# Optimization experiments

Hardware: AMD Instinct MI355X
Metric: run time of the kernel (lower is better)

The kernel has to match this reference:

```python
import jax, jax.numpy as jnp
from jax import lax
import numpy as np

B, S, I, H, O = 4096, 32, 16, 32, 1


def setup_inputs() -> dict:
    key = jax.random.key(0)
    ks = jax.random.split(key, 20)
    sc = 0.1
    inp = {
        "x": jax.random.normal(ks[0], (B, S, I), dtype=jnp.float32),
        "t": jnp.sort(jax.random.uniform(ks[1], (B, S), dtype=jnp.float32), axis=1),
        "gru_Wih": jax.random.normal(ks[2], (3 * H, I), dtype=jnp.float32) * sc,
        "gru_Whh": jax.random.normal(ks[3], (3 * H, H), dtype=jnp.float32) * sc,
        "gru_bih": jax.random.normal(ks[4], (3 * H,), dtype=jnp.float32) * sc,
        "gru_bhh": jax.random.normal(ks[5], (3 * H,), dtype=jnp.float32) * sc,
        "ode_W1": jax.random.normal(ks[6], (64, H), dtype=jnp.float32) * sc,
        "ode_b1": jax.random.normal(ks[7], (64,), dtype=jnp.float32) * sc,
        "ode_W2": jax.random.normal(ks[8], (32, 64), dtype=jnp.float32) * sc,
        "ode_b2": jax.random.normal(ks[9], (32,), dtype=jnp.float32) * sc,
        "ode_W3": jax.random.normal(ks[10], (H, 32), dtype=jnp.float32) * sc,
        "ode_b3": jax.random.normal(ks[11], (H,), dtype=jnp.float32) * sc,
        "fc_W1": jax.random.normal(ks[12], (64, H), dtype=jnp.float32) * sc,
        "fc_b1": jax.random.normal(ks[13], (64,), dtype=jnp.float32) * sc,
        "fc_W2": jax.random.normal(ks[14], (O, 64), dtype=jnp.float32) * sc,
        "fc_b2": jax.random.normal(ks[15], (O,), dtype=jnp.float32) * sc,
        "time_divs": 5,
    }
    return inp


def _forward(x, t, gru_Wih, gru_Whh, gru_bih, gru_bhh,
             ode_W1, ode_b1, ode_W2, ode_b2, ode_W3, ode_b3,
             fc_W1, fc_b1, fc_W2, fc_b2, time_divs):
    n_sub = int(time_divs) - 1  # intervals of the t_eval linspace grid

    def gru_cell(x_t, h):
        gi = x_t @ gru_Wih.T + gru_bih
        gh = h @ gru_Whh.T + gru_bhh
        i_r, i_z, i_n = jnp.split(gi, 3, axis=-1)
        h_r, h_z, h_n = jnp.split(gh, 3, axis=-1)
        r = jax.nn.sigmoid(i_r + h_r)
        z = jax.nn.sigmoid(i_z + h_z)
        n = jnp.tanh(i_n + r * h_n)
        return (1.0 - z) * n + z * h

    def ode_f(y):  # ODEFunc MLP: H -> 64 -> 32 -> H
        h1 = jax.nn.relu(y @ ode_W1.T + ode_b1)
        h2 = jax.nn.relu(h1 @ ode_W2.T + ode_b2)
        return h2 @ ode_W3.T + ode_b3

    def dopri5_step(y, dt):  # dt: (B,1); 5th-order Dormand-Prince step
        k1 = ode_f(y)
        k2 = ode_f(y + dt * (0.2 * k1))
        k3 = ode_f(y + dt * (3 / 40 * k1 + 9 / 40 * k2))
        k4 = ode_f(y + dt * (44 / 45 * k1 - 56 / 15 * k2 + 32 / 9 * k3))
        k5 = ode_f(y + dt * (19372 / 6561 * k1 - 25360 / 2187 * k2
                             + 64448 / 6561 * k3 - 212 / 729 * k4))
        k6 = ode_f(y + dt * (9017 / 3168 * k1 - 355 / 33 * k2 + 46732 / 5247 * k3
                             + 49 / 176 * k4 - 5103 / 18656 * k5))
        return y + dt * (35 / 384 * k1 + 500 / 1113 * k3 + 125 / 192 * k4
                         - 2187 / 6784 * k5 + 11 / 84 * k6)

    def step(carry, inputs):
        h, _ = carry
        x_t, dt = inputs           # x_t: (B,I), dt: (B,)
        out = gru_cell(x_t, h)     # GRU output (also candidate next hidden)
        hi = out
        ddt = (dt / n_sub)[:, None]
        for _ in range(n_sub):     # small fixed substep count, unrolled
            hi = dopri5_step(hi, ddt)
        return (hi, out), None

    bsz = x.shape[0]
    x_seq = jnp.swapaxes(x, 0, 1)[:-1]        # (S-1, B, I)
    dts = (t[:, 1:] - t[:, :-1]).T            # (S-1, B)
    h0 = jnp.zeros((bsz, gru_Whh.shape[1]), dtype=x.dtype)
    (_, out), _ = lax.scan(step, (h0, h0), (x_seq, dts))
    y = jax.nn.relu(out @ fc_W1.T + fc_b1) @ fc_W2.T + fc_b2
    return y


def reference(x, t, gru_Wih, gru_Whh, gru_bih, gru_bhh,
              ode_W1, ode_b1, ode_W2, ode_b2, ode_W3, ode_b3,
              fc_W1, fc_b1, fc_W2, fc_b2, time_divs):
    return _forward(x, t, gru_Wih, gru_Whh, gru_bih, gru_bhh,
                    ode_W1, ode_b1, ode_W2, ode_b2, ode_W3, ode_b3,
                    fc_W1, fc_b1, fc_W2, fc_b2, time_divs)
```

## Files before the change

kernel.cpp:

```cpp
#include <hip/hip_runtime.h>
#include <hip/hip_bf16.h>

#define NB 4096
#define NS 32
#define NI 16
#define NH 32

typedef float f32x2 __attribute__((ext_vector_type(2)));

__device__ __forceinline__ void fence() {
    __builtin_amdgcn_wave_barrier();
    asm volatile("s_waitcnt lgkmcnt(0)" ::: "memory");
    __builtin_amdgcn_wave_barrier();
}

__device__ __forceinline__ float xhsum(float x) {
    auto p = __builtin_amdgcn_permlane32_swap(
        (int)__float_as_uint(x), (int)__float_as_uint(x), false, false);
    return __uint_as_float((unsigned)p[0]) + __uint_as_float((unsigned)p[1]);
}

__device__ __forceinline__ f32x2 pkfma(f32x2 a, f32x2 b, f32x2 c) {
    return __builtin_elementwise_fma(a, b, c);
}

__global__ void __launch_bounds__(256)
__attribute__((amdgpu_waves_per_eu(2, 2)))
odernn_kernel(
    const float* __restrict__ x,
    const float* __restrict__ t,
    const float* __restrict__ gWih,
    const float* __restrict__ gWhh,
    const float* __restrict__ gbih,
    const float* __restrict__ gbhh,
    const float* __restrict__ oW1,
    const float* __restrict__ ob1,
    const float* __restrict__ oW2,
    const float* __restrict__ ob2,
    const float* __restrict__ oW3,
    const float* __restrict__ ob3,
    const float* __restrict__ fW1,
    const float* __restrict__ fb1,
    const float* __restrict__ fW2,
    const float* __restrict__ fb2,
    float* __restrict__ outp)
{
    const int tid  = threadIdx.x;
    const int lane = tid & 63;
    const int wid  = tid >> 6;
    const int b0   = blockIdx.x * 8 + wid * 2;
    const int b1   = b0 + 1;
    const int r    = lane & 31;
    const int hf   = lane >> 5;

    __shared__ float sWr[48 * 32];
    __shared__ float sWz[48 * 32];
    __shared__ float sWnh[32 * 32];
    __shared__ float sWni[16 * 32];
    __shared__ __align__(16) float buf[4][2][64];

    for (int i = tid; i < 48 * 32; i += 256) {
        int c = i >> 5, r0 = i & 31;
        sWr[i] = (c < 16) ? gWih[r0 * 16 + c]        : gWhh[r0 * 32 + (c - 16)];
        sWz[i] = (c < 16) ? gWih[(32 + r0) * 16 + c] : gWhh[(32 + r0) * 32 + (c - 16)];
    }
    for (int i = tid; i < 32 * 32; i += 256) {
        int c = i >> 5, r0 = i & 31;
        sWnh[i] = gWhh[(64 + r0) * 32 + c];
    }
    for (int i = tid; i < 16 * 32; i += 256) {
        int c = i >> 5, r0 = i & 31;
        sWni[i] = gWih[(64 + r0) * 16 + c];
    }
    __syncthreads();

    float* bufw0 = buf[wid][0];
    float* bufw1 = buf[wid][1];
    const float4* bb0 = reinterpret_cast<const float4*>(bufw0);
    const float4* bb1 = reinterpret_cast<const float4*>(bufw1);

    f32x2 w1_0, w1_1, w1_2, w1_3, w1_4, w1_5, w1_6, w1_7,
          w1_8, w1_9, w1_10, w1_11, w1_12, w1_13, w1_14, w1_15;
    f32x2 w2_0, w2_1, w2_2, w2_3, w2_4, w2_5, w2_6, w2_7,
          w2_8, w2_9, w2_10, w2_11, w2_12, w2_13, w2_14, w2_15;
    f32x2 w3_0, w3_1, w3_2, w3_3, w3_4, w3_5, w3_6, w3_7;
    {
        const float4* p1 = reinterpret_cast<const float4*>(oW1) + lane * 8;
        float4 v;
#define LD2(i, dA, dB) { v = p1[i]; dA = f32x2{v.x, v.y}; dB = f32x2{v.z, v.w}; }
        LD2(0, w1_0,  w1_1)  LD2(1, w1_2,  w1_3)
        LD2(2, w1_4,  w1_5)  LD2(3, w1_6,  w1_7)
        LD2(4, w1_8,  w1_9)  LD2(5, w1_10, w1_11)
        LD2(6, w1_12, w1_13) LD2(7, w1_14, w1_15)
#undef LD2
        const float4* p2 = reinterpret_cast<const float4*>(oW2) + r * 16 + hf * 8;
#define LD2(i, dA, dB) { v = p2[i]; dA = f32x2{v.x, v.y}; dB = f32x2{v.z, v.w}; }
        LD2(0, w2_0,  w2_1)  LD2(1, w2_2,  w2_3)
        LD2(2, w2_4,  w2_5)  LD2(3, w2_6,  w2_7)
        LD2(4, w2_8,  w2_9)  LD2(5, w2_10, w2_11)
        LD2(6, w2_12, w2_13) LD2(7, w2_14, w2_15)
#undef LD2
        const float4* p3 = reinterpret_cast<const float4*>(oW3) + r * 8 + hf * 4;
#define LD2(i, dA, dB) { v = p3[i]; dA = f32x2{v.x, v.y}; dB = f32x2{v.z, v.w}; }
        LD2(0, w3_0, w3_1)  LD2(1, w3_2, w3_3)
        LD2(2, w3_4, w3_5)  LD2(3, w3_6, w3_7)
#undef LD2
    }
    const float b1r = ob1[lane];
    const float b2r = ob2[r];
    const float b3r = ob3[r];

    const float brr = gbih[r]      + gbhh[r];
    const float bzz = gbih[32 + r] + gbhh[32 + r];
    const float bin = gbih[64 + r];
    const float bhn = gbhh[64 + r];

    const float* wrp  = &sWr[(hf * 24) * 32 + r];
    const float* wzp  = &sWz[(hf * 24) * 32 + r];
    const float* wnhp = &sWnh[(hf * 16) * 32 + r];
    const float* wnip = &sWni[r];

    auto ode_f2 = [&](float y0, float y1, float& o0, float& o1) {
        bufw0[hf * 32 + r] = y0;
        bufw1[hf * 32 + r] = y1;
        fence();
        f32x2 p0 = f32x2{b1r, 0.0f}, p1a = f32x2{b1r, 0.0f};
#define S1(kk, wA, wB) { float4 c0 = bb0[kk]; float4 c1 = bb1[kk]; \
        p0  = pkfma(wA, f32x2{c0.x, c0.y}, p0);  \
        p0  = pkfma(wB, f32x2{c0.z, c0.w}, p0);  \
        p1a = pkfma(wA, f32x2{c1.x, c1.y}, p1a); \
        p1a = pkfma(wB, f32x2{c1.z, c1.w}, p1a); }
        S1(0, w1_0,  w1_1)  S1(1, w1_2,  w1_3)
        S1(2, w1_4,  w1_5)  S1(3, w1_6,  w1_7)
        S1(4, w1_8,  w1_9)  S1(5, w1_10, w1_11)
        S1(6, w1_12, w1_13) S1(7, w1_14, w1_15)
#undef S1
        float a1_0 = fmaxf(p0.x + p0.y, 0.0f);
        float a1_1 = fmaxf(p1a.x + p1a.y, 0.0f);
        bufw0[lane] = a1_0;
        bufw1[lane] = a1_1;
        fence();
        f32x2 q0 = f32x2{0.0f, 0.0f}, q1 = f32x2{0.0f, 0.0f};
        const int o2 = hf * 8;
#define S2(kk, wA, wB) { float4 c0 = bb0[o2 + kk]; float4 c1 = bb1[o2 + kk]; \
        q0 = pkfma(wA, f32x2{c0.x, c0.y}, q0); \
        q0 = pkfma(wB, f32x2{c0.z, c0.w}, q0); \
        q1 = pkfma(wA, f32x2{c1.x, c1.y}, q1); \
        q1 = pkfma(wB, f32x2{c1.z, c1.w}, q1); }
        S2(0, w2_0,  w2_1)  S2(1, w2_2,  w2_3)
        S2(2, w2_4,  w2_5)  S2(3, w2_6,  w2_7)
        S2(4, w2_8,  w2_9)  S2(5, w2_10, w2_11)
        S2(6, w2_12, w2_13) S2(7, w2_14, w2_15)
#undef S2
        float a2_0 = fmaxf(xhsum(q0.x + q0.y) + b2r, 0.0f);
        float a2_1 = fmaxf(xhsum(q1.x + q1.y) + b2r, 0.0f);
        bufw0[hf * 32 + r] = a2_0;
        bufw1[hf * 32 + r] = a2_1;
        fence();
        f32x2 s0 = f32x2{0.0f, 0.0f}, s1 = f32x2{0.0f, 0.0f};
        const int o3 = hf * 4;
#define S3(kk, wA, wB) { float4 c0 = bb0[o3 + kk]; float4 c1 = bb1[o3 + kk]; \
        s0 = pkfma(wA, f32x2{c0.x, c0.y}, s0); \
        s0 = pkfma(wB, f32x2{c0.z, c0.w}, s0); \
        s1 = pkfma(wA, f32x2{c1.x, c1.y}, s1); \
        s1 = pkfma(wB, f32x2{c1.z, c1.w}, s1); }
        S3(0, w3_0, w3_1)  S3(1, w3_2, w3_3)
        S3(2, w3_4, w3_5)  S3(3, w3_6, w3_7)
#undef S3
        o0 = xhsum(s0.x + s0.y) + b3r;
        o1 = xhsum(s1.x + s1.y) + b3r;
    };

    float hv0 = 0.0f, hv1 = 0.0f;
    float outv0 = 0.0f, outv1 = 0.0f;

    #pragma unroll 1
    for (int s = 0; s < NS - 1; ++s) {
        const float* xrow0 = x + ((size_t)b0 * NS + s) * NI;
        const float* xrow1 = x + ((size_t)b1 * NS + s) * NI;
        if (hf == 0) {
            bufw0[16 + r] = hv0;
            bufw1[16 + r] = hv1;
        } else {
            bufw0[r & 15] = xrow0[r & 15];
            bufw1[r & 15] = xrow1[r & 15];
        }
        fence();

        float ar0 = 0.f, ar1 = 0.f, az0 = 0.f, az1 = 0.f;
        #pragma unroll
        for (int kk = 0; kk < 6; ++kk) {
            float4 c0 = bb0[hf*6 + kk];
            float4 c1 = bb1[hf*6 + kk];
            float w;
            w = wrp[(4*kk  )*32]; ar0 = fmaf(w, c0.x, ar0); ar1 = fmaf(w, c1.x, ar1);
            w = wrp[(4*kk+1)*32]; ar0 = fmaf(w, c0.y, ar0); ar1 = fmaf(w, c1.y, ar1);
            w = wrp[(4*kk+2)*32]; ar0 = fmaf(w, c0.z, ar0); ar1 = fmaf(w, c1.z, ar1);
            w = wrp[(4*kk+3)*32]; ar0 = fmaf(w, c0.w, ar0); ar1 = fmaf(w, c1.w, ar1);
            w = wzp[(4*kk  )*32]; az0 = fmaf(w, c0.x, az0); az1 = fmaf(w, c1.x, az1);
            w = wzp[(4*kk+1)*32]; az0 = fmaf(w, c0.y, az0); az1 = fmaf(w, c1.y, az1);
            w = wzp[(4*kk+2)*32]; az0 = fmaf(w, c0.z, az0); az1 = fmaf(w, c1.z, az1);
            w = wzp[(4*kk+3)*32]; az0 = fmaf(w, c0.w, az0); az1 = fmaf(w, c1.w, az1);
        }
        float in0 = 0.f, in1 = 0.f, hn0 = 0.f, hn1 = 0.f;
        #pragma unroll
        for (int kk = 0; kk < 4; ++kk) {
            float4 c0 = bb0[kk];
            float4 c1 = bb1[kk];
            float w;
            w = wnip[(4*kk  )*32]; in0 = fmaf(w, c0.x, in0); in1 = fmaf(w, c1.x, in1);
            w = wnip[(4*kk+1)*32]; in0 = fmaf(w, c0.y, in0); in1 = fmaf(w, c1.y, in1);
            w = wnip[(4*kk+2)*32]; in0 = fmaf(w, c0.z, in0); in1 = fmaf(w, c1.z, in1);
            w = wnip[(4*kk+3)*32]; in0 = fmaf(w, c0.w, in0); in1 = fmaf(w, c1.w, in1);
        }
        #pragma unroll
        for (int kk = 0; kk < 4; ++kk) {
            float4 c0 = bb0[4 + hf*4 + kk];
            float4 c1 = bb1[4 + hf*4 + kk];
            float w;
            w = wnhp[(4*kk  )*32]; hn0 = fmaf(w, c0.x, hn0); hn1 = fmaf(w, c1.x, hn1);
            w = wnhp[(4*kk+1)*32]; hn0 = fmaf(w, c0.y, hn0); hn1 = fmaf(w, c1.y, hn1);
            w = wnhp[(4*kk+2)*32]; hn0 = fmaf(w, c0.z, hn0); hn1 = fmaf(w, c1.z, hn1);
            w = wnhp[(4*kk+3)*32]; hn0 = fmaf(w, c0.w, hn0); hn1 = fmaf(w, c1.w, hn1);
        }
        ar0 = xhsum(ar0) + brr;  ar1 = xhsum(ar1) + brr;
        az0 = xhsum(az0) + bzz;  az1 = xhsum(az1) + bzz;
        hn0 = xhsum(hn0) + bhn;  hn1 = xhsum(hn1) + bhn;
        in0 += bin;              in1 += bin;

        float rg0 = 1.0f / (1.0f + __expf(-ar0));
        float rg1 = 1.0f / (1.0f + __expf(-ar1));
        float zg0 = 1.0f / (1.0f + __expf(-az0));
        float zg1 = 1.0f / (1.0f + __expf(-az1));
        float ng0 = tanhf(fmaf(rg0, hn0, in0));
        float ng1 = tanhf(fmaf(rg1, hn1, in1));
        outv0 = (1.0f - zg0) * ng0 + zg0 * hv0;
        outv1 = (1.0f - zg1) * ng1 + zg1 * hv1;

        hv0 = outv0;
        hv1 = outv1;
        if (s < NS - 2) {
            const float ddt0 = (t[(size_t)b0 * NS + s + 1] - t[(size_t)b0 * NS + s]) * 0.25f;
            const float ddt1 = (t[(size_t)b1 * NS + s + 1] - t[(size_t)b1 * NS + s]) * 0.25f;
            float hi0 = outv0, hi1 = outv1;
            #pragma unroll 1
            for (int sub = 0; sub < 4; ++sub) {
                float k1_0, k1_1, k2_0, k2_1, k3_0, k3_1,
                      k4_0, k4_1, k5_0, k5_1, k6_0, k6_1;
                ode_f2(hi0, hi1, k1_0, k1_1);
                ode_f2(fmaf(ddt0, 0.2f * k1_0, hi0),
                       fmaf(ddt1, 0.2f * k1_1, hi1), k2_0, k2_1);
                ode_f2(fmaf(ddt0, fmaf((float)(9.0/40.0), k2_0, (float)(3.0/40.0) * k1_0), hi0),
                       fmaf(ddt1, fmaf((float)(9.0/40.0), k2_1, (float)(3.0/40.0) * k1_1), hi1),
                       k3_0, k3_1);
                ode_f2(fmaf(ddt0, fmaf((float)(32.0/9.0), k3_0,
                                  fmaf(-(float)(56.0/15.0), k2_0, (float)(44.0/45.0) * k1_0)), hi0),
                       fmaf(ddt1, fmaf((float)(32.0/9.0), k3_1,
                                  fmaf(-(float)(56.0/15.0), k2_1, (float)(44.0/45.0) * k1_1)), hi1),
                       k4_0, k4_1);
                ode_f2(fmaf(ddt0, fmaf(-(float)(212.0/729.0), k4_0,
                                  fmaf((float)(64448.0/6561.0), k3_0,
                                  fmaf(-(float)(25360.0/2187.0), k2_0, (float)(19372.0/6561.0) * k1_0))), hi0),
                       fmaf(ddt1, fmaf(-(float)(212.0/729.0), k4_1,
                                  fmaf((float)(64448.0/6561.0), k3_1,
                                  fmaf(-(float)(25360.0/2187.0), k2_1, (float)(19372.0/6561.0) * k1_1))), hi1),
                       k5_0, k5_1);
                ode_f2(fmaf(ddt0, fmaf(-(float)(5103.0/18656.0), k5_0,
                                  fmaf((float)(49.0/176.0), k4_0,
                                  fmaf((float)(46732.0/5247.0), k3_0,
                                  fmaf(-(float)(355.0/33.0), k2_0, (float)(9017.0/3168.0) * k1_0)))), hi0),
                       fmaf(ddt1, fmaf(-(float)(5103.0/18656.0), k5_1,
                                  fmaf((float)(49.0/176.0), k4_1,
                                  fmaf((float)(46732.0/5247.0), k3_1,
                                  fmaf(-(float)(355.0/33.0), k2_1, (float)(9017.0/3168.0) * k1_1)))), hi1),
                       k6_0, k6_1);
                hi0 = fmaf(ddt0, fmaf((float)(11.0/84.0), k6_0,
                                 fmaf(-(float)(2187.0/6784.0), k5_0,
                                 fmaf((float)(125.0/192.0), k4_0,
                                 fmaf((float)(500.0/1113.0), k3_0, (float)(35.0/384.0) * k1_0)))), hi0);
                hi1 = fmaf(ddt1, fmaf((float)(11.0/84.0), k6_1,
                                 fmaf(-(float)(2187.0/6784.0), k5_1,
                                 fmaf((float)(125.0/192.0), k4_1,
                                 fmaf((float)(500.0/1113.0), k3_1, (float)(35.0/384.0) * k1_1)))), hi1);
            }
            hv0 = hi0;
            hv1 = hi1;
        }
    }

    bufw0[hf * 32 + r] = outv0;
    bufw1[hf * 32 + r] = outv1;
    fence();
    f32x2 acc0 = f32x2{fb1[lane], 0.0f};
    f32x2 acc1h = f32x2{fb1[lane], 0.0f};
    {
        const float4* fw = reinterpret_cast<const float4*>(fW1) + lane * 8;
        #pragma unroll
        for (int kk = 0; kk < 8; ++kk) {
            float4 wv = fw[kk];
            float4 c0 = bb0[kk];
            float4 c1 = bb1[kk];
            acc0  = pkfma(f32x2{wv.x, wv.y}, f32x2{c0.x, c0.y}, acc0);
            acc0  = pkfma(f32x2{wv.z, wv.w}, f32x2{c0.z, c0.w}, acc0);
            acc1h = pkfma(f32x2{wv.x, wv.y}, f32x2{c1.x, c1.y}, acc1h);
            acc1h = pkfma(f32x2{wv.z, wv.w}, f32x2{c1.z, c1.w}, acc1h);
        }
    }
    float fw2v = fW2[lane];
    float pa = fmaxf(acc0.x + acc0.y, 0.0f) * fw2v;
    float pb = fmaxf(acc1h.x + acc1h.y, 0.0f) * fw2v;
    #pragma unroll
    for (int m = 1; m < 64; m <<= 1) {
        pa += __shfl_xor(pa, m, 64);
        pb += __shfl_xor(pb, m, 64);
    }
    if (lane == 0) {
        float bias = fb2[0];
        outp[b0] = pa + bias;
        outp[b1] = pb + bias;
    }
}

extern "C" void kernel_launch(void* const* d_in, const int* in_sizes, int n_in,
                              void* d_out, int out_size, void* d_ws, size_t ws_size,
                              hipStream_t stream) {
    (void)in_sizes; (void)n_in; (void)d_ws; (void)ws_size; (void)out_size;
    odernn_kernel<<<dim3(NB / 8), dim3(256), 0, stream>>>(
        (const float*)d_in[0],  (const float*)d_in[1],
        (const float*)d_in[2],  (const float*)d_in[3],
        (const float*)d_in[4],  (const float*)d_in[5],
        (const float*)d_in[6],  (const float*)d_in[7],
        (const float*)d_in[8],  (const float*)d_in[9],
        (const float*)d_in[10], (const float*)d_in[11],
        (const float*)d_in[12], (const float*)d_in[13],
        (const float*)d_in[14], (const float*)d_in[15],
        (float*)d_out);
}
```

Measured before the change: 692.8 us.

## Repartition ODE MLP across lanes with packed two-output state and permlane reductions

The ODE MLP work is redistributed so each lane holds two output neurons packed into f32x2. The K dimension is split across half-waves and quarter-waves, and partial sums are combined with permlane16/permlane32 swaps. The RK stage combinations now run as packed FMAs on the two-element state, which removes redundant per-lane scalar stage arithmetic. The cost is extra cross-lane reductions and an LDS round trip to re-layout the hidden state before the ODE loop.

```diff
diff --git a/kernel.cpp b/kernel.cpp
--- a/kernel.cpp
+++ b/kernel.cpp
@@ -14,14 +14,22 @@
     __builtin_amdgcn_wave_barrier();
 }
 
-__device__ __forceinline__ float xhsum(float x) {
+__device__ __forceinline__ float xh32(float x) {
     auto p = __builtin_amdgcn_permlane32_swap(
         (int)__float_as_uint(x), (int)__float_as_uint(x), false, false);
     return __uint_as_float((unsigned)p[0]) + __uint_as_float((unsigned)p[1]);
 }
+__device__ __forceinline__ float xh16(float x) {
+    auto p = __builtin_amdgcn_permlane16_swap(
+        (int)__float_as_uint(x), (int)__float_as_uint(x), false, false);
+    return __uint_as_float((unsigned)p[0]) + __uint_as_float((unsigned)p[1]);
+}
 
 __device__ __forceinline__ f32x2 pkfma(f32x2 a, f32x2 b, f32x2 c) {
     return __builtin_elementwise_fma(a, b, c);
+}
+__device__ __forceinline__ f32x2 pfm(float a, f32x2 b, f32x2 c) {
+    return __builtin_elementwise_fma(f32x2{a, a}, b, c);
 }
 
 __global__ void __launch_bounds__(256)
@@ -52,6 +60,8 @@
     const int b1   = b0 + 1;
     const int r    = lane & 31;
     const int hf   = lane >> 5;
+    const int p    = lane & 15;
+    const int q    = lane >> 4;
 
     __shared__ float sWr[48 * 32];
     __shared__ float sWz[48 * 32];
@@ -81,34 +91,49 @@
 
     f32x2 w1_0, w1_1, w1_2, w1_3, w1_4, w1_5, w1_6, w1_7,
           w1_8, w1_9, w1_10, w1_11, w1_12, w1_13, w1_14, w1_15;
+    {
+        const float4* A = reinterpret_cast<const float4*>(oW1 + r * 32 + hf * 16);
+        const float4* B = reinterpret_cast<const float4*>(oW1 + (r + 32) * 32 + hf * 16);
+        float4 a, bq;
+#define LW(kk, d0, d1, d2, d3) { a = A[kk]; bq = B[kk]; \
+        d0 = f32x2{a.x, bq.x}; d1 = f32x2{a.y, bq.y}; \
+        d2 = f32x2{a.z, bq.z}; d3 = f32x2{a.w, bq.w}; }
+        LW(0, w1_0, w1_1, w1_2,  w1_3)
+        LW(1, w1_4, w1_5, w1_6,  w1_7)
+        LW(2, w1_8, w1_9, w1_10, w1_11)
+        LW(3, w1_12, w1_13, w1_14, w1_15)
+#undef LW
+    }
     f32x2 w2_0, w2_1, w2_2, w2_3, w2_4, w2_5, w2_6, w2_7,
           w2_8, w2_9, w2_10, w2_11, w2_12, w2_13, w2_14, w2_15;
+    {
+        const float4* A = reinterpret_cast<const float4*>(oW2 + p * 64 + q * 16);
+        const float4* B = reinterpret_cast<const float4*>(oW2 + (p + 16) * 64 + q * 16);
+        float4 a, bq;
+#define LW(kk, d0, d1, d2, d3) { a = A[kk]; bq = B[kk]; \
+        d0 = f32x2{a.x, bq.x}; d1 = f32x2{a.y, bq.y}; \
+        d2 = f32x2{a.z, bq.z}; d3 = f32x2{a.w, bq.w}; }
+        LW(0, w2_0, w2_1, w2_2,  w2_3)
+        LW(1, w2_4, w2_5, w2_6,  w2_7)
+        LW(2, w2_8, w2_9, w2_10, w2_11)
+        LW(3, w2_12, w2_13, w2_14, w2_15)
+#undef LW
+    }
     f32x2 w3_0, w3_1, w3_2, w3_3, w3_4, w3_5, w3_6, w3_7;
     {
-        const float4* p1 = reinterpret_cast<const float4*>(oW1) + lane * 8;
-        float4 v;
-#define LD2(i, dA, dB) { v = p1[i]; dA = f32x2{v.x, v.y}; dB = f32x2{v.z, v.w}; }
-        LD2(0, w1_0,  w1_1)  LD2(1, w1_2,  w1_3)
-        LD2(2, w1_4,  w1_5)  LD2(3, w1_6,  w1_7)
-        LD2(4, w1_8,  w1_9)  LD2(5, w1_10, w1_11)
-        LD2(6, w1_12, w1_13) LD2(7, w1_14, w1_15)
-#undef LD2
-        const float4* p2 = reinterpret_cast<const float4*>(oW2) + r * 16 + hf * 8;
-#define LD2(i, dA, dB) { v = p2[i]; dA = f32x2{v.x, v.y}; dB = f32x2{v.z, v.w}; }
-        LD2(0, w2_0,  w2_1)  LD2(1, w2_2,  w2_3)
-        LD2(2, w2_4,  w2_5)  LD2(3, w2_6,  w2_7)
-        LD2(4, w2_8,  w2_9)  LD2(5, w2_10, w2_11)
-        LD2(6, w2_12, w2_13) LD2(7, w2_14, w2_15)
-#undef LD2
-        const float4* p3 = reinterpret_cast<const float4*>(oW3) + r * 8 + hf * 4;
-#define LD2(i, dA, dB) { v = p3[i]; dA = f32x2{v.x, v.y}; dB = f32x2{v.z, v.w}; }
-        LD2(0, w3_0, w3_1)  LD2(1, w3_2, w3_3)
-        LD2(2, w3_4, w3_5)  LD2(3, w3_6, w3_7)
-#undef LD2
-    }
-    const float b1r = ob1[lane];
-    const float b2r = ob2[r];
-    const float b3r = ob3[r];
+        const float4* A = reinterpret_cast<const float4*>(oW3 + p * 32 + q * 8);
+        const float4* B = reinterpret_cast<const float4*>(oW3 + (p + 16) * 32 + q * 8);
+        float4 a, bq;
+#define LW(kk, d0, d1, d2, d3) { a = A[kk]; bq = B[kk]; \
+        d0 = f32x2{a.x, bq.x}; d1 = f32x2{a.y, bq.y}; \
+        d2 = f32x2{a.z, bq.z}; d3 = f32x2{a.w, bq.w}; }
+        LW(0, w3_0, w3_1, w3_2, w3_3)
+        LW(1, w3_4, w3_5, w3_6, w3_7)
+#undef LW
+    }
+    const f32x2 b1pk = f32x2{ob1[r], ob1[r + 32]};
+    const f32x2 b2pk = f32x2{ob2[p], ob2[p + 16]};
+    const f32x2 b3pk = f32x2{ob3[p], ob3[p + 16]};
 
     const float brr = gbih[r]      + gbhh[r];
     const float bzz = gbih[32 + r] + gbhh[32 + r];
@@ -120,78 +145,90 @@
     const float* wnhp = &sWnh[(hf * 16) * 32 + r];
     const float* wnip = &sWni[r];
 
-    auto ode_f2 = [&](float y0, float y1, float& o0, float& o1) {
-        bufw0[hf * 32 + r] = y0;
-        bufw1[hf * 32 + r] = y1;
+    const int hf4  = hf * 4;
+    const int q4   = q * 4;
+    const int q2   = q * 2;
+    const int wsel = (q & 1) << 4;
+
+    auto ode_f2 = [&](f32x2 y0, f32x2 y1, f32x2& o0, f32x2& o1) {
+        bufw0[p + wsel] = (q & 1) ? y0.y : y0.x;
+        bufw1[p + wsel] = (q & 1) ? y1.y : y1.x;
         fence();
-        f32x2 p0 = f32x2{b1r, 0.0f}, p1a = f32x2{b1r, 0.0f};
-#define S1(kk, wA, wB) { float4 c0 = bb0[kk]; float4 c1 = bb1[kk]; \
-        p0  = pkfma(wA, f32x2{c0.x, c0.y}, p0);  \
-        p0  = pkfma(wB, f32x2{c0.z, c0.w}, p0);  \
-        p1a = pkfma(wA, f32x2{c1.x, c1.y}, p1a); \
-        p1a = pkfma(wB, f32x2{c1.z, c1.w}, p1a); }
-        S1(0, w1_0,  w1_1)  S1(1, w1_2,  w1_3)
-        S1(2, w1_4,  w1_5)  S1(3, w1_6,  w1_7)
-        S1(4, w1_8,  w1_9)  S1(5, w1_10, w1_11)
-        S1(6, w1_12, w1_13) S1(7, w1_14, w1_15)
-#undef S1
-        float a1_0 = fmaxf(p0.x + p0.y, 0.0f);
-        float a1_1 = fmaxf(p1a.x + p1a.y, 0.0f);
-        bufw0[lane] = a1_0;
-        bufw1[lane] = a1_1;
+        f32x2 A0 = f32x2{0.f, 0.f}, A1 = f32x2{0.f, 0.f};
+#define S1M(kk, wA, wB, wC, wD) { \
+        float4 c0 = bb0[hf4 + kk], c1 = bb1[hf4 + kk]; \
+        A0 = pkfma(wA, f32x2{c0.x, c0.x}, A0); A1 = pkfma(wA, f32x2{c1.x, c1.x}, A1); \
+        A0 = pkfma(wB, f32x2{c0.y, c0.y}, A0); A1 = pkfma(wB, f32x2{c1.y, c1.y}, A1); \
+        A0 = pkfma(wC, f32x2{c0.z, c0.z}, A0); A1 = pkfma(wC, f32x2{c1.z, c1.z}, A1); \
+        A0 = pkfma(wD, f32x2{c0.w, c0.w}, A0); A1 = pkfma(wD, f32x2{c1.w, c1.w}, A1); }
+        S1M(0, w1_0,  w1_1,  w1_2,  w1_3)
+        S1M(1, w1_4,  w1_5,  w1_6,  w1_7)
+        S1M(2, w1_8,  w1_9,  w1_10, w1_11)
+        S1M(3, w1_12, w1_13, w1_14, w1_15)
+#undef S1M
+        f32x2 h10 = f32x2{fmaxf(xh32(A0.x) + b1pk.x, 0.f),
+                          fmaxf(xh32(A0.y) + b1pk.y, 0.f)};
+        f32x2 h11 = f32x2{fmaxf(xh32(A1.x) + b1pk.x, 0.f),
+                          fmaxf(xh32(A1.y) + b1pk.y, 0.f)};
+        bufw0[lane] = hf ? h10.y : h10.x;
+        bufw1[lane] = hf ? h11.y : h11.x;
         fence();
-        f32x2 q0 = f32x2{0.0f, 0.0f}, q1 = f32x2{0.0f, 0.0f};
-        const int o2 = hf * 8;
-#define S2(kk, wA, wB) { float4 c0 = bb0[o2 + kk]; float4 c1 = bb1[o2 + kk]; \
-        q0 = pkfma(wA, f32x2{c0.x, c0.y}, q0); \
-        q0 = pkfma(wB, f32x2{c0.z, c0.w}, q0); \
-        q1 = pkfma(wA, f32x2{c1.x, c1.y}, q1); \
-        q1 = pkfma(wB, f32x2{c1.z, c1.w}, q1); }
-        S2(0, w2_0,  w2_1)  S2(1, w2_2,  w2_3)
-        S2(2, w2_4,  w2_5)  S2(3, w2_6,  w2_7)
-        S2(4, w2_8,  w2_9)  S2(5, w2_10, w2_11)
-        S2(6, w2_12, w2_13) S2(7, w2_14, w2_15)
-#undef S2
-        float a2_0 = fmaxf(xhsum(q0.x + q0.y) + b2r, 0.0f);
-        float a2_1 = fmaxf(xhsum(q1.x + q1.y) + b2r, 0.0f);
-        bufw0[hf * 32 + r] = a2_0;
-        bufw1[hf * 32 + r] = a2_1;
+        f32x2 B0 = f32x2{0.f, 0.f}, B1 = f32x2{0.f, 0.f};
+#define S2M(kk, wA, wB, wC, wD) { \
+        float4 c0 = bb0[q4 + kk], c1 = bb1[q4 + kk]; \
+        B0 = pkfma(wA, f32x2{c0.x, c0.x}, B0); B1 = pkfma(wA, f32x2{c1.x, c1.x}, B1); \
+        B0 = pkfma(wB, f32x2{c0.y, c0.y}, B0); B1 = pkfma(wB, f32x2{c1.y, c1.y}, B1); \
+        B0 = pkfma(wC, f32x2{c0.z, c0.z}, B0); B1 = pkfma(wC, f32x2{c1.z, c1.z}, B1); \
+        B0 = pkfma(wD, f32x2{c0.w, c0.w}, B0); B1 = pkfma(wD, f32x2{c1.w, c1.w}, B1); }
+        S2M(0, w2_0,  w2_1,  w2_2,  w2_3)
+        S2M(1, w2_4,  w2_5,  w2_6,  w2_7)
+        S2M(2, w2_8,  w2_9,  w2_10, w2_11)
+        S2M(3, w2_12, w2_13, w2_14, w2_15)
+#undef S2M
+        f32x2 h20 = f32x2{fmaxf(xh32(xh16(B0.x)) + b2pk.x, 0.f),
+                          fmaxf(xh32(xh16(B0.y)) + b2pk.y, 0.f)};
+        f32x2 h21 = f32x2{fmaxf(xh32(xh16(B1.x)) + b2pk.x, 0.f),
+                          fmaxf(xh32(xh16(B1.y)) + b2pk.y, 0.f)};
+        bufw0[p + wsel] = (q & 1) ? h20.y : h20.x;
+        bufw1[p + wsel] = (q & 1) ? h21.y : h21.x;
         fence();
-        f32x2 s0 = f32x2{0.0f, 0.0f}, s1 = f32x2{0.0f, 0.0f};
-        const int o3 = hf * 4;
-#define S3(kk, wA, wB) { float4 c0 = bb0[o3 + kk]; float4 c1 = bb1[o3 + kk]; \
-        s0 = pkfma(wA, f32x2{c0.x, c0.y}, s0); \
-        s0 = pkfma(wB, f32x2{c0.z, c0.w}, s0); \
-        s1 = pkfma(wA, f32x2{c1.x, c1.y}, s1); \
-        s1 = pkfma(wB, f32x2{c1.z, c1.w}, s1); }
-        S3(0, w3_0, w3_1)  S3(1, w3_2, w3_3)
-        S3(2, w3_4, w3_5)  S3(3, w3_6, w3_7)
-#undef S3
-        o0 = xhsum(s0.x + s0.y) + b3r;
-        o1 = xhsum(s1.x + s1.y) + b3r;
+        f32x2 C0 = f32x2{0.f, 0.f}, C1 = f32x2{0.f, 0.f};
+#define S3M(kk, wA, wB, wC, wD) { \
+        float4 c0 = bb0[q2 + kk], c1 = bb1[q2 + kk]; \
+        C0 = pkfma(wA, f32x2{c0.x, c0.x}, C0); C1 = pkfma(wA, f32x2{c1.x, c1.x}, C1); \
+        C0 = pkfma(wB, f32x2{c0.y, c0.y}, C0); C1 = pkfma(wB, f32x2{c1.y, c1.y}, C1); \
+        C0 = pkfma(wC, f32x2{c0.z, c0.z}, C0); C1 = pkfma(wC, f32x2{c1.z, c1.z}, C1); \
+        C0 = pkfma(wD, f32x2{c0.w, c0.w}, C0); C1 = pkfma(wD, f32x2{c1.w, c1.w}, C1); }
+        S3M(0, w3_0, w3_1, w3_2, w3_3)
+        S3M(1, w3_4, w3_5, w3_6, w3_7)
+#undef S3M
+        o0 = f32x2{xh32(xh16(C0.x)) + b3pk.x, xh32(xh16(C0.y)) + b3pk.y};
+        o1 = f32x2{xh32(xh16(C1.x)) + b3pk.x, xh32(xh16(C1.y)) + b3pk.y};
     };
 
-    float hv0 = 0.0f, hv1 = 0.0f;
-    float outv0 = 0.0f, outv1 = 0.0f;
+    f32x2 hv0 = f32x2{0.f, 0.f}, hv1 = f32x2{0.f, 0.f};
+    float outv0 = 0.f, outv1 = 0.f;
 
     #pragma unroll 1
     for (int s = 0; s < NS - 1; ++s) {
         const float* xrow0 = x + ((size_t)b0 * NS + s) * NI;
         const float* xrow1 = x + ((size_t)b1 * NS + s) * NI;
-        if (hf == 0) {
-            bufw0[16 + r] = hv0;
-            bufw1[16 + r] = hv1;
-        } else {
-            bufw0[r & 15] = xrow0[r & 15];
-            bufw1[r & 15] = xrow1[r & 15];
-        }
+        float xv0 = xrow0[p];
+        float xv1 = xrow1[p];
+        int   sa  = p + ((q == 1) ? 16 : (q == 2) ? 32 : 0);
+        float sv0 = (q == 1) ? hv0.x : (q == 2) ? hv0.y : xv0;
+        float sv1 = (q == 1) ? hv1.x : (q == 2) ? hv1.y : xv1;
+        bufw0[sa] = sv0;
+        bufw1[sa] = sv1;
         fence();
+        float hvX0 = bufw0[16 + r];
+        float hvX1 = bufw1[16 + r];
 
         float ar0 = 0.f, ar1 = 0.f, az0 = 0.f, az1 = 0.f;
         #pragma unroll
         for (int kk = 0; kk < 6; ++kk) {
-            float4 c0 = bb0[hf*6 + kk];
-            float4 c1 = bb1[hf*6 + kk];
+            float4 c0 = bb0[hf * 6 + kk];
+            float4 c1 = bb1[hf * 6 + kk];
             float w;
             w = wrp[(4*kk  )*32]; ar0 = fmaf(w, c0.x, ar0); ar1 = fmaf(w, c1.x, ar1);
             w = wrp[(4*kk+1)*32]; ar0 = fmaf(w, c0.y, ar0); ar1 = fmaf(w, c1.y, ar1);
@@ -215,18 +252,18 @@
         }
         #pragma unroll
         for (int kk = 0; kk < 4; ++kk) {
-            float4 c0 = bb0[4 + hf*4 + kk];
-            float4 c1 = bb1[4 + hf*4 + kk];
+            float4 c0 = bb0[4 + hf * 4 + kk];
+            float4 c1 = bb1[4 + hf * 4 + kk];
             float w;
             w = wnhp[(4*kk  )*32]; hn0 = fmaf(w, c0.x, hn0); hn1 = fmaf(w, c1.x, hn1);
             w = wnhp[(4*kk+1)*32]; hn0 = fmaf(w, c0.y, hn0); hn1 = fmaf(w, c1.y, hn1);
             w = wnhp[(4*kk+2)*32]; hn0 = fmaf(w, c0.z, hn0); hn1 = fmaf(w, c1.z, hn1);
             w = wnhp[(4*kk+3)*32]; hn0 = fmaf(w, c0.w, hn0); hn1 = fmaf(w, c1.w, hn1);
         }
-        ar0 = xhsum(ar0) + brr;  ar1 = xhsum(ar1) + brr;
-        az0 = xhsum(az0) + bzz;  az1 = xhsum(az1) + bzz;
-        hn0 = xhsum(hn0) + bhn;  hn1 = xhsum(hn1) + bhn;
-        in0 += bin;              in1 += bin;
+        ar0 = xh32(ar0) + brr;  ar1 = xh32(ar1) + brr;
+        az0 = xh32(az0) + bzz;  az1 = xh32(az1) + bzz;
+        hn0 = xh32(hn0) + bhn;  hn1 = xh32(hn1) + bhn;
+        in0 += bin;             in1 += bin;
 
         float rg0 = 1.0f / (1.0f + __expf(-ar0));
         float rg1 = 1.0f / (1.0f + __expf(-ar1));
@@ -234,54 +271,56 @@
         float zg1 = 1.0f / (1.0f + __expf(-az1));
         float ng0 = tanhf(fmaf(rg0, hn0, in0));
         float ng1 = tanhf(fmaf(rg1, hn1, in1));
-        outv0 = (1.0f - zg0) * ng0 + zg0 * hv0;
-        outv1 = (1.0f - zg1) * ng1 + zg1 * hv1;
-
-        hv0 = outv0;
-        hv1 = outv1;
+        outv0 = (1.0f - zg0) * ng0 + zg0 * hvX0;
+        outv1 = (1.0f - zg1) * ng1 + zg1 * hvX1;
+
         if (s < NS - 2) {
             const float ddt0 = (t[(size_t)b0 * NS + s + 1] - t[(size_t)b0 * NS + s]) * 0.25f;
             const float ddt1 = (t[(size_t)b1 * NS + s + 1] - t[(size_t)b1 * NS + s]) * 0.25f;
-            float hi0 = outv0, hi1 = outv1;
+            bufw0[r] = outv0;
+            bufw1[r] = outv1;
+            fence();
+            f32x2 hi0 = f32x2{bufw0[p], bufw0[p + 16]};
+            f32x2 hi1 = f32x2{bufw1[p], bufw1[p + 16]};
             #pragma unroll 1
             for (int sub = 0; sub < 4; ++sub) {
-                float k1_0, k1_1, k2_0, k2_1, k3_0, k3_1,
+                f32x2 k1_0, k1_1, k2_0, k2_1, k3_0, k3_1,
                       k4_0, k4_1, k5_0, k5_1, k6_0, k6_1;
                 ode_f2(hi0, hi1, k1_0, k1_1);
-                ode_f2(fmaf(ddt0, 0.2f * k1_0, hi0),
-                       fmaf(ddt1, 0.2f * k1_1, hi1), k2_0, k2_1);
-                ode_f2(fmaf(ddt0, fmaf((float)(9.0/40.0), k2_0, (float)(3.0/40.0) * k1_0), hi0),
-                       fmaf(ddt1, fmaf((float)(9.0/40.0), k2_1, (float)(3.0/40.0) * k1_1), hi1),
+                ode_f2(pfm(ddt0, 0.2f * k1_0, hi0),
+                       pfm(ddt1, 0.2f * k1_1, hi1), k2_0, k2_1);
+                ode_f2(pfm(ddt0, pfm((float)(9.0/40.0), k2_0, (float)(3.0/40.0) * k1_0), hi0),
+                       pfm(ddt1, pfm((float)(9.0/40.0), k2_1, (float)(3.0/40.0) * k1_1), hi1),
                        k3_0, k3_1);
-                ode_f2(fmaf(ddt0, fmaf((float)(32.0/9.0), k3_0,
-                                  fmaf(-(float)(56.0/15.0), k2_0, (float)(44.0/45.0) * k1_0)), hi0),
-                       fmaf(ddt1, fmaf((float)(32.0/9.0), k3_1,
-                                  fmaf(-(float)(56.0/15.0), k2_1, (float)(44.0/45.0) * k1_1)), hi1),
+                ode_f2(pfm(ddt0, pfm((float)(32.0/9.0), k3_0,
+                                 pfm(-(float)(56.0/15.0), k2_0, (float)(44.0/45.0) * k1_0)), hi0),
+                       pfm(ddt1, pfm((float)(32.0/9.0), k3_1,
+                                 pfm(-(float)(56.0/15.0), k2_1, (float)(44.0/45.0) * k1_1)), hi1),
                        k4_0, k4_1);
-                ode_f2(fmaf(ddt0, fmaf(-(float)(212.0/729.0), k4_0,
-                                  fmaf((float)(64448.0/6561.0), k3_0,
-                                  fmaf(-(float)(25360.0/2187.0), k2_0, (float)(19372.0/6561.0) * k1_0))), hi0),
-                       fmaf(ddt1, fmaf(-(float)(212.0/729.0), k4_1,
-                                  fmaf((float)(64448.0/6561.0), k3_1,
-                                  fmaf(-(float)(25360.0/2187.0), k2_1, (float)(19372.0/6561.0) * k1_1))), hi1),
+                ode_f2(pfm(ddt0, pfm(-(float)(212.0/729.0), k4_0,
+                                 pfm((float)(64448.0/6561.0), k3_0,
+                                 pfm(-(float)(25360.0/2187.0), k2_0, (float)(19372.0/6561.0) * k1_0))), hi0),
+                       pfm(ddt1, pfm(-(float)(212.0/729.0), k4_1,
+                                 pfm((float)(64448.0/6561.0), k3_1,
+                                 pfm(-(float)(25360.0/2187.0), k2_1, (float)(19372.0/6561.0) * k1_1))), hi1),
                        k5_0, k5_1);
-                ode_f2(fmaf(ddt0, fmaf(-(float)(5103.0/18656.0), k5_0,
-                                  fmaf((float)(49.0/176.0), k4_0,
-                                  fmaf((float)(46732.0/5247.0), k3_0,
-                                  fmaf(-(float)(355.0/33.0), k2_0, (float)(9017.0/3168.0) * k1_0)))), hi0),
-                       fmaf(ddt1, fmaf(-(float)(5103.0/18656.0), k5_1,
-                                  fmaf((float)(49.0/176.0), k4_1,
-                                  fmaf((float)(46732.0/5247.0), k3_1,
-                                  fmaf(-(float)(355.0/33.0), k2_1, (float)(9017.0/3168.0) * k1_1)))), hi1),
+                ode_f2(pfm(ddt0, pfm(-(float)(5103.0/18656.0), k5_0,
+                                 pfm((float)(49.0/176.0), k4_0,
+                                 pfm((float)(46732.0/5247.0), k3_0,
+                                 pfm(-(float)(355.0/33.0), k2_0, (float)(9017.0/3168.0) * k1_0)))), hi0),
+                       pfm(ddt1, pfm(-(float)(5103.0/18656.0), k5_1,
+                                 pfm((float)(49.0/176.0), k4_1,
+                                 pfm((float)(46732.0/5247.0), k3_1,
+                                 pfm(-(float)(355.0/33.0), k2_1, (float)(9017.0/3168.0) * k1_1)))), hi1),
                        k6_0, k6_1);
-                hi0 = fmaf(ddt0, fmaf((float)(11.0/84.0), k6_0,
-                                 fmaf(-(float)(2187.0/6784.0), k5_0,
-                                 fmaf((float)(125.0/192.0), k4_0,
-                                 fmaf((float)(500.0/1113.0), k3_0, (float)(35.0/384.0) * k1_0)))), hi0);
-                hi1 = fmaf(ddt1, fmaf((float)(11.0/84.0), k6_1,
-                                 fmaf(-(float)(2187.0/6784.0), k5_1,
-                                 fmaf((float)(125.0/192.0), k4_1,
-                                 fmaf((float)(500.0/1113.0), k3_1, (float)(35.0/384.0) * k1_1)))), hi1);
+                hi0 = pfm(ddt0, pfm((float)(11.0/84.0), k6_0,
+                                pfm(-(float)(2187.0/6784.0), k5_0,
+                                pfm((float)(125.0/192.0), k4_0,
+                                pfm((float)(500.0/1113.0), k3_0, (float)(35.0/384.0) * k1_0)))), hi0);
+                hi1 = pfm(ddt1, pfm((float)(11.0/84.0), k6_1,
+                                pfm(-(float)(2187.0/6784.0), k5_1,
+                                pfm((float)(125.0/192.0), k4_1,
+                                pfm((float)(500.0/1113.0), k3_1, (float)(35.0/384.0) * k1_1)))), hi1);
             }
             hv0 = hi0;
             hv1 = hi1;
@@ -291,7 +330,7 @@
     bufw0[hf * 32 + r] = outv0;
     bufw1[hf * 32 + r] = outv1;
     fence();
-    f32x2 acc0 = f32x2{fb1[lane], 0.0f};
+    f32x2 acc0  = f32x2{fb1[lane], 0.0f};
     f32x2 acc1h = f32x2{fb1[lane], 0.0f};
     {
         const float4* fw = reinterpret_cast<const float4*>(fW1) + lane * 8;
```

After: 722.4 us. +4.3%, slower.
